# Kernel tuning notes

Measured on AMD Instinct MI355X. Metric: run time of the kernel, lower is better.

Reference implementation:

```python
import jax, jax.numpy as jnp
import numpy as np

EMBED_DIM = 1024
NUM_HEADS = 16
HEAD_DIM = EMBED_DIM // NUM_HEADS


def setup_inputs() -> dict:
    key = jax.random.key(0)
    ks = jax.random.split(key, 5)
    T, B, E = 2048, 2, EMBED_DIM
    s = 1.0 / np.sqrt(E)
    return {
        "x": jax.random.normal(ks[0], (T, B, E), jnp.float32),
        "wq": jax.random.normal(ks[1], (E, E), jnp.float32) * s,
        "bq": jnp.zeros((E,), jnp.float32),
        "wk": jax.random.normal(ks[2], (E, E), jnp.float32) * s,
        "bk": jnp.zeros((E,), jnp.float32),
        "wv": jax.random.normal(ks[3], (E, E), jnp.float32) * s,
        "bv": jnp.zeros((E,), jnp.float32),
        "wo": jax.random.normal(ks[4], (E, E), jnp.float32) * s,
        "bo": jnp.zeros((E,), jnp.float32),
    }


def reference(x, wq, bq, wk, bk, wv, bv, wo, bo):
    # x: [T, B, E] (Time x Batch x Channel), self-attention: query = key = value = x
    T, B, E = x.shape
    H, D = NUM_HEADS, HEAD_DIM
    scaling = D ** -0.5
    # Linear projections (torch Linear: y = x @ W.T + b)
    q = (jnp.einsum('tbe,fe->tbf', x, wq) + bq) * scaling
    k = jnp.einsum('tbe,fe->tbf', x, wk) + bk
    v = jnp.einsum('tbe,fe->tbf', x, wv) + bv
    # reshape to [B*H, T, D] equivalent -> use [B, H, T, D]
    q = q.reshape(T, B, H, D).transpose(1, 2, 0, 3)  # [B,H,T,D]
    k = k.reshape(T, B, H, D).transpose(1, 2, 0, 3)
    v = v.reshape(T, B, H, D).transpose(1, 2, 0, 3)
    # scores: [B,H,T,S], fp32 softmax
    scores = jnp.einsum('bhtd,bhsd->bhts', q, k)
    probs = jax.nn.softmax(scores.astype(jnp.float32), axis=-1).astype(x.dtype)
    attn = jnp.einsum('bhts,bhsd->bhtd', probs, v)  # [B,H,T,D]
    attn = attn.transpose(2, 0, 1, 3).reshape(T, B, E)
    out = jnp.einsum('tbe,fe->tbf', attn, wo) + bo
    return out
```

## Files before the change

### kernel.cpp

```cpp
#include <hip/hip_runtime.h>
#include <cstddef>
#include <cstdint>

#define T_DIM 2048
#define E_DIM 1024
#define M_DIM 4096

typedef __attribute__((ext_vector_type(8))) short short8;
typedef __attribute__((ext_vector_type(8))) _Float16 half8;
typedef __attribute__((ext_vector_type(4))) _Float16 half4;
typedef __attribute__((ext_vector_type(4))) float f32x4;

__device__ __forceinline__ short f16_bits(float v) {
  return __builtin_bit_cast(short, (_Float16)v);
}
__device__ __forceinline__ unsigned int pk2(float a, float b) {
  return __builtin_bit_cast(unsigned int, __builtin_amdgcn_cvt_pkrtz(a, b));
}
__device__ __forceinline__ half8 h8(short8 s) { return __builtin_bit_cast(half8, s); }

__device__ __forceinline__ void gl_lds16(const short* g, const short* l) {
  __builtin_amdgcn_global_load_lds(
      (const __attribute__((address_space(1))) unsigned int*)g,
      (__attribute__((address_space(3))) unsigned int*)l, 16, 0, 0);
}

__global__ __launch_bounds__(256) void convert_all(
    const float* __restrict__ x, const float* __restrict__ wq,
    const float* __restrict__ wk, const float* __restrict__ wv,
    const float* __restrict__ wo,
    short* __restrict__ xh, short* __restrict__ wqh, short* __restrict__ wkh,
    short* __restrict__ wvh, short* __restrict__ woh)
{
  const int bid = blockIdx.x;
  const float* in; short* hi; int base;
  if (bid < 4096)      { in = x;  hi = xh;  base = 0;    }
  else if (bid < 5120) { in = wq; hi = wqh; base = 4096; }
  else if (bid < 6144) { in = wk; hi = wkh; base = 5120; }
  else if (bid < 7168) { in = wv; hi = wvh; base = 6144; }
  else                 { in = wo; hi = woh; base = 7168; }
  const int i = (bid - base) * 256 + threadIdx.x;
  float4 v = ((const float4*)in)[i];
  uint2 p;
  p.x = (unsigned short)f16_bits(v.x) | ((unsigned int)(unsigned short)f16_bits(v.y) << 16);
  p.y = (unsigned short)f16_bits(v.z) | ((unsigned int)(unsigned short)f16_bits(v.w) << 16);
  ((uint2*)hi)[i] = p;
}

__global__ __launch_bounds__(256) void gemm_qkv(
    const short* __restrict__ xh,
    const short* __restrict__ wqh, const short* __restrict__ wkh,
    const short* __restrict__ wvh,
    const float* __restrict__ bq, const float* __restrict__ bk,
    const float* __restrict__ bv,
    short* __restrict__ qo, short* __restrict__ ko, short* __restrict__ vto)
{
  __shared__ __align__(16) short smem[128 * 64 * 2];
  short* Ah = smem;
  short* Wh = smem + 8192;
  const int tid = threadIdx.x;
  const int lane = tid & 63;
  const int w = tid >> 6;
  const int quad = lane >> 4;
  const int l15 = lane & 15;
  const int sel = blockIdx.x >> 3;
  const int n0 = (blockIdx.x & 7) * 128;
  const int m0 = blockIdx.y * 128;

  const short* wsel = sel == 0 ? wqh : sel == 1 ? wkh : wvh;
  const float* bias = sel == 0 ? bq : sel == 1 ? bk : bv;
  const float scale = sel == 0 ? 0.125f * 1.44269504088896f : 1.0f;

  const short* gsrc = (w < 2) ? xh : wsel;
  short* lbuf = (w < 2) ? Ah : Wh;
  const int rbase = (w < 2) ? m0 : n0;
  const int lrow8 = lane >> 3;
  const int gph8 = lane & 7;
  const int kg = (gph8 - lrow8) & 7;

  f32x4 zero = {0.f, 0.f, 0.f, 0.f};
  f32x4 acc[4][4];
#pragma unroll
  for (int i = 0; i < 4; ++i)
#pragma unroll
    for (int j = 0; j < 4; ++j) acc[i][j] = zero;

  const int wm = w & 1, wn = w >> 1;

  for (int k0 = 0; k0 < E_DIM; k0 += 64) {
    __syncthreads();
#pragma unroll
    for (int jj = 0; jj < 8; ++jj) {
      int j = (w & 1) * 8 + jj;
      int r = j * 8 + lrow8;
      gl_lds16(gsrc + (size_t)(rbase + r) * E_DIM + k0 + kg * 8, lbuf + j * 512);
    }
    __syncthreads();
#pragma unroll
    for (int ks = 0; ks < 2; ++ks) {
      short8 ahf[4];
#pragma unroll
      for (int i = 0; i < 4; ++i) {
        int r = wm * 64 + i * 16 + l15;
        ahf[i] = *(const short8*)&Ah[r * 64 + ((ks * 4 + quad + r) & 7) * 8];
      }
#pragma unroll
      for (int j = 0; j < 4; ++j) {
        int r = wn * 64 + j * 16 + l15;
        short8 bhf = *(const short8*)&Wh[r * 64 + ((ks * 4 + quad + r) & 7) * 8];
#pragma unroll
        for (int i = 0; i < 4; ++i)
          acc[i][j] = __builtin_amdgcn_mfma_f32_16x16x32_f16(h8(ahf[i]), h8(bhf), acc[i][j], 0, 0, 0);
      }
    }
  }

  if (sel < 2) {
#pragma unroll
    for (int j = 0; j < 4; ++j) {
      const int gc = n0 + wn * 64 + j * 16 + l15;
      const float bb = bias[gc];
      const int h = gc >> 6, d = gc & 63;
      short* dst = sel == 0 ? qo : ko;
#pragma unroll
      for (int i = 0; i < 4; ++i)
#pragma unroll
        for (int reg = 0; reg < 4; ++reg) {
          const int gm = m0 + wm * 64 + i * 16 + quad * 4 + reg;
          const float val = (acc[i][j][reg] + bb) * scale;
          const int t = gm >> 1, b = gm & 1;
          dst[((size_t)(b * 16 + h) * T_DIM + t) * 64 + d] = f16_bits(val);
        }
    }
  } else {
    short* Tb = smem;
    const int by = blockIdx.y;
#pragma unroll
    for (int R = 0; R < 2; ++R) {
      __syncthreads();
      if (wn == R) {
#pragma unroll
        for (int j = 0; j < 4; ++j) {
          const int nl = j * 16 + l15;
          const int gc = n0 + R * 64 + nl;
          const float bb = bias[gc];
#pragma unroll
          for (int i = 0; i < 4; ++i) {
            const int tp = wm * 32 + i * 8 + quad * 2;
            unsigned int lo = pk2(acc[i][j][0] + bb, acc[i][j][2] + bb);
            unsigned int hi = pk2(acc[i][j][1] + bb, acc[i][j][3] + bb);
            const int g0 = tp >> 3;
            const int sub = tp & 7;
            *(unsigned int*)&Tb[nl * 128 + ((g0 + nl) & 15) * 8 + sub] = lo;
            *(unsigned int*)&Tb[nl * 128 + ((g0 + 8 + nl) & 15) * 8 + sub] = hi;
          }
        }
      }
      __syncthreads();
#pragma unroll
      for (int ii = 0; ii < 4; ++ii) {
        const int n = w * 16 + ii * 4 + quad;
        const int g = (l15 - n) & 15;
        short8 vvec = *(const short8*)&Tb[n * 128 + l15 * 8];
        const int gc = n0 + R * 64 + n;
        const int h = gc >> 6, d = gc & 63;
        const int b = g >> 3;
        const int t = by * 64 + (g & 7) * 8;
        *(short8*)&vto[((size_t)(b * 16 + h) * 64 + d) * T_DIM + t] = vvec;
      }
    }
  }
}

__global__ __launch_bounds__(256) void gemm_out(
    const short* __restrict__ attn, const short* __restrict__ woh,
    float* __restrict__ p0, float* __restrict__ p1)
{
  __shared__ __align__(16) short smem[128 * 64 * 2];
  short* Ah = smem;
  short* Wh = smem + 8192;
  const int tid = threadIdx.x;
  const int lane = tid & 63;
  const int w = tid >> 6;
  const int quad = lane >> 4;
  const int l15 = lane & 15;
  const int n0 = blockIdx.x * 128;
  const int m0 = blockIdx.y * 128;
  const int z = blockIdx.z;
  float* part = z ? p1 : p0;

  const short* gsrc = (w < 2) ? attn : woh;
  short* lbuf = (w < 2) ? Ah : Wh;
  const int rbase = (w < 2) ? m0 : n0;
  const int lrow8 = lane >> 3;
  const int gph8 = lane & 7;
  const int kg = (gph8 - lrow8) & 7;

  f32x4 zero = {0.f, 0.f, 0.f, 0.f};
  f32x4 acc[4][4];
#pragma unroll
  for (int i = 0; i < 4; ++i)
#pragma unroll
    for (int j = 0; j < 4; ++j) acc[i][j] = zero;

  const int wm = w & 1, wn = w >> 1;

  for (int k0 = z * 512; k0 < z * 512 + 512; k0 += 64) {
    __syncthreads();
#pragma unroll
    for (int jj = 0; jj < 8; ++jj) {
      int j = (w & 1) * 8 + jj;
      int r = j * 8 + lrow8;
      gl_lds16(gsrc + (size_t)(rbase + r) * E_DIM + k0 + kg * 8, lbuf + j * 512);
    }
    __syncthreads();
#pragma unroll
    for (int ks = 0; ks < 2; ++ks) {
      short8 ahf[4];
#pragma unroll
      for (int i = 0; i < 4; ++i) {
        int r = wm * 64 + i * 16 + l15;
        ahf[i] = *(const short8*)&Ah[r * 64 + ((ks * 4 + quad + r) & 7) * 8];
      }
#pragma unroll
      for (int j = 0; j < 4; ++j) {
        int r = wn * 64 + j * 16 + l15;
        short8 bhf = *(const short8*)&Wh[r * 64 + ((ks * 4 + quad + r) & 7) * 8];
#pragma unroll
        for (int i = 0; i < 4; ++i)
          acc[i][j] = __builtin_amdgcn_mfma_f32_16x16x32_f16(h8(ahf[i]), h8(bhf), acc[i][j], 0, 0, 0);
      }
    }
  }

#pragma unroll
  for (int j = 0; j < 4; ++j) {
    const int gc = n0 + wn * 64 + j * 16 + l15;
#pragma unroll
    for (int i = 0; i < 4; ++i)
#pragma unroll
      for (int reg = 0; reg < 4; ++reg) {
        const int gm = m0 + wm * 64 + i * 16 + quad * 4 + reg;
        part[(size_t)gm * E_DIM + gc] = acc[i][j][reg];
      }
  }
}

__global__ __launch_bounds__(256) void add_bias(
    const float* __restrict__ p0, const float* __restrict__ p1,
    const float* __restrict__ bo, float* __restrict__ out)
{
  const int i = blockIdx.x * 256 + threadIdx.x;
  const int col = (i * 4) & (E_DIM - 1);
  float4 a = ((const float4*)p0)[i];
  float4 b = ((const float4*)p1)[i];
  float4 c = *(const float4*)&bo[col];
  float4 o;
  o.x = a.x + b.x + c.x; o.y = a.y + b.y + c.y;
  o.z = a.z + b.z + c.z; o.w = a.w + b.w + c.w;
  ((float4*)out)[i] = o;
}

__global__ __launch_bounds__(256, 2) void attn_mfma(
    const short* __restrict__ q, const short* __restrict__ k,
    const short* __restrict__ vt, short* __restrict__ attn)
{
  __shared__ __align__(16) short SMEM[32768];
  __shared__ float l_red[4][128];
  short* Qs = SMEM;
  short* KV = SMEM + 8192;

  const int tid = threadIdx.x;
  const int lane = tid & 63;
  const int w = tid >> 6;
  const int quad = lane >> 4;
  const int l15 = lane & 15;
  const int bhid = blockIdx.y;
  const int b = bhid >> 4, h = bhid & 15;
  const int t0 = blockIdx.x * 128;

  const short* qb = q + (size_t)bhid * T_DIM * 64;
  const short* kb = k + (size_t)bhid * T_DIM * 64;
  const short* vb = vt + (size_t)bhid * 64 * T_DIM;

  const int lrow8 = lane >> 3;
  const int gph8 = lane & 7;

#pragma unroll
  for (int jj = 0; jj < 4; ++jj) {
    int j = w * 4 + jj;
    int r = j * 8 + lrow8;
    int gl = (gph8 - (r >> 1)) & 7;
    gl_lds16(qb + (size_t)(t0 + r) * 64 + gl * 8, Qs + j * 512);
  }

  const int kg = (gph8 - lrow8) & 7;
  const int vd = lane >> 1, vh = lane & 1;
#pragma unroll
  for (int c0 = 0; c0 < 2; ++c0) {
    short* slot = KV + c0 * 8192 + w * 2048;
    const int sg = c0 * 64 + w * 16;
    gl_lds16(kb + (size_t)(sg + lrow8) * 64 + kg * 8, slot);
    gl_lds16(kb + (size_t)(sg + lrow8 + 8) * 64 + kg * 8, slot + 512);
    gl_lds16(vb + (size_t)vd * T_DIM + sg + vh * 8, slot + 1024);
    gl_lds16(vb + (size_t)(vd + 32) * T_DIM + sg + vh * 8, slot + 1536);
  }
  __syncthreads();

  short8 qa[8][2];
#pragma unroll
  for (int qbk = 0; qbk < 8; ++qbk)
#pragma unroll
    for (int st = 0; st < 2; ++st) {
      int r = qbk * 16 + l15;
      int idx = r * 64 + (((st * 4 + quad) + (r >> 1)) & 7) * 8;
      qa[qbk][st] = *(const short8*)&Qs[idx];
    }

  f32x4 zero = {0.f, 0.f, 0.f, 0.f};
  f32x4 acc[4][8];
  float l_part[8];
#pragma unroll
  for (int d = 0; d < 4; ++d)
#pragma unroll
    for (int qb2 = 0; qb2 < 8; ++qb2) acc[d][qb2] = zero;
#pragma unroll
  for (int i = 0; i < 8; ++i) l_part[i] = 0.f;

  for (int c = 0; c < 32; ++c) {
    if (c >= 2) {
      if (c == 31) __builtin_amdgcn_s_waitcnt(0x0F70);
      else         __builtin_amdgcn_s_waitcnt(0x0F74);
    }
    const short* slot = KV + (c % 3) * 8192 + w * 2048;

    short8 kf[2];
#pragma unroll
    for (int st = 0; st < 2; ++st)
      kf[st] = *(const short8*)&slot[l15 * 64 + (((st * 4 + quad) + l15) & 7) * 8];
    uint2 vfu[4];
#pragma unroll
    for (int dblk = 0; dblk < 4; ++dblk)
      vfu[dblk] = *(const uint2*)&slot[1024 + (dblk * 16 + l15) * 16 + quad * 4];

    if (c < 30) {
      short* nslot = KV + ((c + 2) % 3) * 8192 + w * 2048;
      const int sg = (c + 2) * 64 + w * 16;
      gl_lds16(kb + (size_t)(sg + lrow8) * 64 + kg * 8, nslot);
      gl_lds16(kb + (size_t)(sg + lrow8 + 8) * 64 + kg * 8, nslot + 512);
      gl_lds16(vb + (size_t)vd * T_DIM + sg + vh * 8, nslot + 1024);
      gl_lds16(vb + (size_t)(vd + 32) * T_DIM + sg + vh * 8, nslot + 1536);
    }

    uint2 pb[8];
#pragma unroll
    for (int qbk = 0; qbk < 8; ++qbk) {
      f32x4 s = zero;
      s = __builtin_amdgcn_mfma_f32_16x16x32_f16(h8(kf[0]), h8(qa[qbk][0]), s, 0, 0, 0);
      s = __builtin_amdgcn_mfma_f32_16x16x32_f16(h8(kf[1]), h8(qa[qbk][1]), s, 0, 0, 0);
      float p0 = __builtin_amdgcn_exp2f(s[0]);
      float p1 = __builtin_amdgcn_exp2f(s[1]);
      float p2 = __builtin_amdgcn_exp2f(s[2]);
      float p3 = __builtin_amdgcn_exp2f(s[3]);
      l_part[qbk] += (p0 + p1) + (p2 + p3);
      pb[qbk].x = pk2(p0, p1);
      pb[qbk].y = pk2(p2, p3);
    }

#pragma unroll
    for (int dblk = 0; dblk < 4; ++dblk) {
      half4 va = __builtin_bit_cast(half4, vfu[dblk]);
#pragma unroll
      for (int qbk = 0; qbk < 8; ++qbk)
        acc[dblk][qbk] = __builtin_amdgcn_mfma_f32_16x16x16f16(
            va, __builtin_bit_cast(half4, pb[qbk]), acc[dblk][qbk], 0, 0, 0);
    }
  }

#pragma unroll
  for (int qbk = 0; qbk < 8; ++qbk) {
    float l = l_part[qbk];
    l += __shfl_xor(l, 16);
    l += __shfl_xor(l, 32);
    if (quad == 0) l_red[w][qbk * 16 + l15] = l;
  }

  f32x4* Osc = (f32x4*)SMEM;
  __syncthreads();
  if (w & 1) {
    f32x4* dst = Osc + (w >> 1) * 2048;
#pragma unroll
    for (int dblk = 0; dblk < 4; ++dblk)
#pragma unroll
      for (int qbk = 0; qbk < 8; ++qbk)
        dst[(dblk * 8 + qbk) * 64 + lane] = acc[dblk][qbk];
  }
  __syncthreads();
  if (!(w & 1)) {
    f32x4* src = Osc + (w >> 1) * 2048;
#pragma unroll
    for (int dblk = 0; dblk < 4; ++dblk)
#pragma unroll
      for (int qbk = 0; qbk < 8; ++qbk) {
        f32x4 t = src[(dblk * 8 + qbk) * 64 + lane];
        acc[dblk][qbk][0] += t[0]; acc[dblk][qbk][1] += t[1];
        acc[dblk][qbk][2] += t[2]; acc[dblk][qbk][3] += t[3];
      }
  }
  __syncthreads();
  if (w == 2) {
#pragma unroll
    for (int dblk = 0; dblk < 4; ++dblk)
#pragma unroll
      for (int qbk = 0; qbk < 8; ++qbk)
        Osc[(dblk * 8 + qbk) * 64 + lane] = acc[dblk][qbk];
  }
  __syncthreads();
  if (w == 0) {
#pragma unroll
    for (int qbk = 0; qbk < 8; ++qbk) {
      const int qq = qbk * 16 + l15;
      const float lsum = l_red[0][qq] + l_red[1][qq] + l_red[2][qq] + l_red[3][qq];
      const float inv = 1.f / lsum;
      const int t = t0 + qq;
      const size_t mrow = (size_t)(t * 2 + b) * E_DIM;
#pragma unroll
      for (int dblk = 0; dblk < 4; ++dblk) {
        f32x4 t4 = Osc[(dblk * 8 + qbk) * 64 + lane];
        float a0 = acc[dblk][qbk][0] + t4[0];
        float a1 = acc[dblk][qbk][1] + t4[1];
        float a2 = acc[dblk][qbk][2] + t4[2];
        float a3 = acc[dblk][qbk][3] + t4[3];
        uint2 ov;
        ov.x = pk2(a0 * inv, a1 * inv);
        ov.y = pk2(a2 * inv, a3 * inv);
        *(uint2*)&attn[mrow + h * 64 + dblk * 16 + quad * 4] = ov;
      }
    }
  }
}

extern "C" void kernel_launch(void* const* d_in, const int* in_sizes, int n_in,
                              void* d_out, int out_size, void* d_ws, size_t ws_size,
                              hipStream_t stream)
{
  const float* x  = (const float*)d_in[0];
  const float* wq = (const float*)d_in[1];
  const float* bq = (const float*)d_in[2];
  const float* wk = (const float*)d_in[3];
  const float* bk = (const float*)d_in[4];
  const float* wv = (const float*)d_in[5];
  const float* bv = (const float*)d_in[6];
  const float* wo = (const float*)d_in[7];
  const float* bo = (const float*)d_in[8];
  float* out = (float*)d_out;

  short* ws = (short*)d_ws;
  const size_t M4 = (size_t)M_DIM * E_DIM;
  const size_t M1 = (size_t)E_DIM * E_DIM;
  short* aws  = ws;
  short* woh  = aws + M4;
  short* xh   = woh + M1;
  short* wqh  = xh + M4;
  short* wkh  = wqh + M1;
  short* wvh  = wkh + M1;
  short* qws  = wvh + M1;
  short* kws  = qws + M4;
  short* vtws = kws + M4;
  float* part0 = (float*)xh;
  float* part1 = part0 + M4;

  convert_all<<<8192, 256, 0, stream>>>(x, wq, wk, wv, wo, xh, wqh, wkh, wvh, woh);
  gemm_qkv<<<dim3(24, 32), 256, 0, stream>>>(xh, wqh, wkh, wvh, bq, bk, bv,
                                             qws, kws, vtws);
  attn_mfma<<<dim3(16, 32), 256, 0, stream>>>(qws, kws, vtws, aws);
  gemm_out<<<dim3(8, 32, 2), 256, 0, stream>>>(aws, woh, part0, part1);
  add_bias<<<4096, 256, 0, stream>>>(part0, part1, bo, out);
}
```

Baseline: 204.0 us.

## Fuse split-K output GEMM reduction and bias into one 512-thread kernel

```diff
diff --git a/kernel.cpp b/kernel.cpp
--- a/kernel.cpp
+++ b/kernel.cpp
@@ -172,26 +172,26 @@
   }
 }
 
-__global__ __launch_bounds__(256) void gemm_out(
+__global__ __launch_bounds__(512, 4) void gemm_out_fused(
     const short* __restrict__ attn, const short* __restrict__ woh,
-    float* __restrict__ p0, float* __restrict__ p1)
+    const float* __restrict__ bo, float* __restrict__ out)
 {
-  __shared__ __align__(16) short smem[128 * 64 * 2];
-  short* Ah = smem;
-  short* Wh = smem + 8192;
+  __shared__ __align__(16) short smem[32768];
   const int tid = threadIdx.x;
   const int lane = tid & 63;
   const int w = tid >> 6;
+  const int g = w >> 2;
+  const int wg = w & 3;
   const int quad = lane >> 4;
   const int l15 = lane & 15;
   const int n0 = blockIdx.x * 128;
   const int m0 = blockIdx.y * 128;
-  const int z = blockIdx.z;
-  float* part = z ? p1 : p0;
-
-  const short* gsrc = (w < 2) ? attn : woh;
-  short* lbuf = (w < 2) ? Ah : Wh;
-  const int rbase = (w < 2) ? m0 : n0;
+
+  short* Ah = smem + g * 16384;
+  short* Wh = Ah + 8192;
+  const short* gsrc = (wg < 2) ? attn : woh;
+  short* lbuf = (wg < 2) ? Ah : Wh;
+  const int rbase = (wg < 2) ? m0 : n0;
   const int lrow8 = lane >> 3;
   const int gph8 = lane & 7;
   const int kg = (gph8 - lrow8) & 7;
@@ -203,13 +203,13 @@
 #pragma unroll
     for (int j = 0; j < 4; ++j) acc[i][j] = zero;
 
-  const int wm = w & 1, wn = w >> 1;
-
-  for (int k0 = z * 512; k0 < z * 512 + 512; k0 += 64) {
+  const int wm = wg & 1, wn = wg >> 1;
+
+  for (int k0 = g * 512; k0 < g * 512 + 512; k0 += 64) {
     __syncthreads();
 #pragma unroll
     for (int jj = 0; jj < 8; ++jj) {
-      int j = (w & 1) * 8 + jj;
+      int j = (wg & 1) * 8 + jj;
       int r = j * 8 + lrow8;
       gl_lds16(gsrc + (size_t)(rbase + r) * E_DIM + k0 + kg * 8, lbuf + j * 512);
     }
@@ -233,32 +233,34 @@
     }
   }
 
-#pragma unroll
-  for (int j = 0; j < 4; ++j) {
-    const int gc = n0 + wn * 64 + j * 16 + l15;
+  __syncthreads();
+  f32x4* Osc = (f32x4*)smem;
+  if (g == 1) {
+    f32x4* dst = Osc + wg * 1024;
 #pragma unroll
     for (int i = 0; i < 4; ++i)
 #pragma unroll
-      for (int reg = 0; reg < 4; ++reg) {
-        const int gm = m0 + wm * 64 + i * 16 + quad * 4 + reg;
-        part[(size_t)gm * E_DIM + gc] = acc[i][j][reg];
-      }
-  }
-}
-
-__global__ __launch_bounds__(256) void add_bias(
-    const float* __restrict__ p0, const float* __restrict__ p1,
-    const float* __restrict__ bo, float* __restrict__ out)
-{
-  const int i = blockIdx.x * 256 + threadIdx.x;
-  const int col = (i * 4) & (E_DIM - 1);
-  float4 a = ((const float4*)p0)[i];
-  float4 b = ((const float4*)p1)[i];
-  float4 c = *(const float4*)&bo[col];
-  float4 o;
-  o.x = a.x + b.x + c.x; o.y = a.y + b.y + c.y;
-  o.z = a.z + b.z + c.z; o.w = a.w + b.w + c.w;
-  ((float4*)out)[i] = o;
+      for (int j = 0; j < 4; ++j)
+        dst[(i * 4 + j) * 64 + lane] = acc[i][j];
+  }
+  __syncthreads();
+  if (g == 0) {
+    f32x4* src = Osc + wg * 1024;
+#pragma unroll
+    for (int j = 0; j < 4; ++j) {
+      const int gc = n0 + wn * 64 + j * 16 + l15;
+      const float bb = bo[gc];
+#pragma unroll
+      for (int i = 0; i < 4; ++i) {
+        f32x4 t = src[(i * 4 + j) * 64 + lane];
+#pragma unroll
+        for (int reg = 0; reg < 4; ++reg) {
+          const int gm = m0 + wm * 64 + i * 16 + quad * 4 + reg;
+          out[(size_t)gm * E_DIM + gc] = acc[i][j][reg] + t[reg] + bb;
+        }
+      }
+    }
+  }
 }
 
 __global__ __launch_bounds__(256, 2) void attn_mfma(
@@ -410,10 +412,17 @@
   __syncthreads();
   if (w == 2) {
 #pragma unroll
-    for (int dblk = 0; dblk < 4; ++dblk)
+    for (int d2 = 0; d2 < 2; ++d2)
 #pragma unroll
       for (int qbk = 0; qbk < 8; ++qbk)
-        Osc[(dblk * 8 + qbk) * 64 + lane] = acc[dblk][qbk];
+        Osc[(d2 * 8 + qbk) * 64 + lane] = acc[d2][qbk];
+  }
+  if (w == 0) {
+#pragma unroll
+    for (int d2 = 0; d2 < 2; ++d2)
+#pragma unroll
+      for (int qbk = 0; qbk < 8; ++qbk)
+        Osc[1024 + (d2 * 8 + qbk) * 64 + lane] = acc[2 + d2][qbk];
   }
   __syncthreads();
   if (w == 0) {
@@ -425,16 +434,30 @@
       const int t = t0 + qq;
       const size_t mrow = (size_t)(t * 2 + b) * E_DIM;
 #pragma unroll
-      for (int dblk = 0; dblk < 4; ++dblk) {
-        f32x4 t4 = Osc[(dblk * 8 + qbk) * 64 + lane];
-        float a0 = acc[dblk][qbk][0] + t4[0];
-        float a1 = acc[dblk][qbk][1] + t4[1];
-        float a2 = acc[dblk][qbk][2] + t4[2];
-        float a3 = acc[dblk][qbk][3] + t4[3];
+      for (int d2 = 0; d2 < 2; ++d2) {
+        f32x4 t4 = Osc[(d2 * 8 + qbk) * 64 + lane];
         uint2 ov;
-        ov.x = pk2(a0 * inv, a1 * inv);
-        ov.y = pk2(a2 * inv, a3 * inv);
-        *(uint2*)&attn[mrow + h * 64 + dblk * 16 + quad * 4] = ov;
+        ov.x = pk2((acc[d2][qbk][0] + t4[0]) * inv, (acc[d2][qbk][1] + t4[1]) * inv);
+        ov.y = pk2((acc[d2][qbk][2] + t4[2]) * inv, (acc[d2][qbk][3] + t4[3]) * inv);
+        *(uint2*)&attn[mrow + h * 64 + d2 * 16 + quad * 4] = ov;
+      }
+    }
+  }
+  if (w == 2) {
+#pragma unroll
+    for (int qbk = 0; qbk < 8; ++qbk) {
+      const int qq = qbk * 16 + l15;
+      const float lsum = l_red[0][qq] + l_red[1][qq] + l_red[2][qq] + l_red[3][qq];
+      const float inv = 1.f / lsum;
+      const int t = t0 + qq;
+      const size_t mrow = (size_t)(t * 2 + b) * E_DIM;
+#pragma unroll
+      for (int d2 = 0; d2 < 2; ++d2) {
+        f32x4 t4 = Osc[1024 + (d2 * 8 + qbk) * 64 + lane];
+        uint2 ov;
+        ov.x = pk2((acc[2 + d2][qbk][0] + t4[0]) * inv, (acc[2 + d2][qbk][1] + t4[1]) * inv);
+        ov.y = pk2((acc[2 + d2][qbk][2] + t4[2]) * inv, (acc[2 + d2][qbk][3] + t4[3]) * inv);
+        *(uint2*)&attn[mrow + h * 64 + (2 + d2) * 16 + quad * 4] = ov;
       }
     }
   }
@@ -467,13 +490,10 @@
   short* qws  = wvh + M1;
   short* kws  = qws + M4;
   short* vtws = kws + M4;
-  float* part0 = (float*)xh;
-  float* part1 = part0 + M4;
 
   convert_all<<<8192, 256, 0, stream>>>(x, wq, wk, wv, wo, xh, wqh, wkh, wvh, woh);
   gemm_qkv<<<dim3(24, 32), 256, 0, stream>>>(xh, wqh, wkh, wvh, bq, bk, bv,
                                              qws, kws, vtws);
   attn_mfma<<<dim3(16, 32), 256, 0, stream>>>(qws, kws, vtws, aws);
-  gemm_out<<<dim3(8, 32, 2), 256, 0, stream>>>(aws, woh, part0, part1);
-  add_bias<<<4096, 256, 0, stream>>>(part0, part1, bo, out);
-}
+  gemm_out_fused<<<dim3(8, 32), 512, 0, stream>>>(aws, woh, bo, out);
+}
```

After: 191.9 us. -5.9%, faster.
